# Kernel tuning notes

Measured on AMD Instinct MI355X. Metric: run time of the kernel, lower is better.

## Reference

```python
import jax, jax.numpy as jnp
import numpy as np
from jax import lax

B, C_IN, C_OUT, KK, KS = 8, 32, 64, 4, 3
D, H, W = 32, 64, 64
PAD = 1

def setup_inputs() -> dict:
    key = jax.random.key(0)
    ks = jax.random.split(key, 12)
    s = 0.02
    return {
        "x": jax.random.normal(ks[0], (B, C_IN, D, H, W), jnp.float32),
        # K candidate conv kernels and biases
        "weight": jax.random.normal(ks[1], (KK, C_OUT, C_IN, KS, KS, KS), jnp.float32) * s,
        "cbias": jnp.zeros((KK, C_OUT), jnp.float32),
        "temperature": jnp.float32(34.0),
        # attention key path: BN(affine, eval-mode) -> GELU -> 1x1 conv (linear)
        "bn1_g": jnp.ones((C_IN,), jnp.float32),
        "bn1_b": jnp.zeros((C_IN,), jnp.float32),
        "w1": jax.random.normal(ks[2], (C_IN, C_IN), jnp.float32) * s,
        "b1": jnp.zeros((C_IN,), jnp.float32),
        "bn2_g": jnp.ones((C_IN,), jnp.float32),
        "bn2_b": jnp.zeros((C_IN,), jnp.float32),
        "w2": jax.random.normal(ks[3], (C_IN, C_IN), jnp.float32) * s,
        "b2": jnp.zeros((C_IN,), jnp.float32),
        "bn3_g": jnp.ones((C_IN,), jnp.float32),
        "bn3_b": jnp.zeros((C_IN,), jnp.float32),
        "w3": jax.random.normal(ks[4], (KK, C_IN), jnp.float32) * s,
        "b3": jnp.zeros((KK,), jnp.float32),
    }

def _attention(p, temperature, bn1_g, bn1_b, w1, b1, bn2_g, bn2_b, w2, b2, bn3_g, bn3_b, w3, b3):
    # p: [B, C] pooled features. 1x1x1 convs on 1x1x1 maps == linear layers.
    gelu = lambda t: jax.nn.gelu(t, approximate=False)  # torch nn.GELU default is erf
    a = gelu(p * bn1_g + bn1_b)          # BN (eval: rm=0, rv=1) + GELU
    a = a @ w1.T + b1
    a = gelu(a * bn2_g + bn2_b)
    a = a @ w2.T + b2
    a = a + p                            # ResidualLayer (plain add)
    a = a * bn3_g + bn3_b
    logits = a @ w3.T + b3               # [B, K]
    return jax.nn.softmax(logits / temperature, axis=1)

def reference(x, weight, cbias, temperature, bn1_g, bn1_b, w1, b1,
              bn2_g, bn2_b, w2, b2, bn3_g, bn3_b, w3, b3):
    # x: [B, C_in, D, H, W]
    p = x.mean(axis=(2, 3, 4))  # AdaptiveAvgPool3d(1)
    attn = _attention(p, temperature, bn1_g, bn1_b, w1, b1,
                      bn2_g, bn2_b, w2, b2, bn3_g, bn3_b, w3, b3)  # [B, K]
    # per-sample aggregated kernels / bias
    agg_w = jnp.einsum('bk,koidhw->boidhw', attn, weight)  # [B, O, I, k, k, k]
    agg_b = attn @ cbias                                    # [B, O]
    # grouped-conv trick (groups=B) == per-sample conv3d -> vmap over batch
    def conv1(xi, wi):
        return lax.conv_general_dilated(
            xi[None], wi, window_strides=(1, 1, 1),
            padding=[(PAD, PAD)] * 3,
            dimension_numbers=('NCDHW', 'OIDHW', 'NCDHW'))[0]
    out = jax.vmap(conv1)(x, agg_w)  # [B, O, D, H, W]
    return out + agg_b[:, :, None, None, None]
```

## Files before the change

kernel.cpp:

```cpp
#include <hip/hip_runtime.h>
#include <hip/hip_bf16.h>
#include <math.h>

#define B_   8
#define CIN  32
#define COUT 64
#define KK_  4
#define DD   32
#define HH   64
#define WW   64
#define HW   (HH*WW)
#define DHW  (DD*HH*WW)

typedef __attribute__((ext_vector_type(8)))  short bf16x8;
typedef __attribute__((ext_vector_type(16))) float f32x16;

__device__ __forceinline__ unsigned short f2bf(float f) {
    union { float f; unsigned int u; } v; v.f = f;
    return (unsigned short)((v.u + 0x7FFFu + ((v.u >> 16) & 1u)) >> 16);
}
__device__ __forceinline__ float bf2f(unsigned short s) {
    union { unsigned int u; float f; } v; v.u = ((unsigned int)s) << 16;
    return v.f;
}
__device__ __forceinline__ void gll16(const void* g, void* l) {
    __builtin_amdgcn_global_load_lds(
        (const __attribute__((address_space(1))) void*)g,
        (__attribute__((address_space(3))) void*)l, 16, 0, 0);
}

__global__ __launch_bounds__(256) void transpose_kernel(const float* __restrict__ x,
                                                        unsigned short* __restrict__ xt) {
    const int t = threadIdx.x;
    const int r = t >> 6, w = t & 63;
    const int h = (blockIdx.x << 2) + r;
    const int d = blockIdx.y, b = blockIdx.z;

    const float* xb = x + (size_t)b*CIN*DHW + (size_t)d*HW + (size_t)h*WW + w;
    unsigned int packed[CIN/2];
    #pragma unroll
    for (int c2 = 0; c2 < CIN/2; ++c2) {
        unsigned int lo = f2bf(xb[(size_t)(2*c2)   * DHW]);
        unsigned int hi = f2bf(xb[(size_t)(2*c2+1) * DHW]);
        packed[c2] = lo | (hi << 16);
    }
    char* row = (char*)xt + (size_t)((b*DD + d)*HH + h) * 4096;
    #pragma unroll
    for (int q = 0; q < 4; ++q) {
        uint4 v = make_uint4(packed[4*q], packed[4*q+1], packed[4*q+2], packed[4*q+3]);
        *(uint4*)(row + q*1024 + (((w << 4)) ^ (q << 4))) = v;
    }
}

__global__ __launch_bounds__(256) void pool2_kernel(const unsigned short* __restrict__ xt,
                                                    float* __restrict__ pblk) {
    const int t = threadIdx.x;
    const int oct = t >> 6, wi = t & 63;
    const int d = blockIdx.x, b = blockIdx.y;
    const char* base = (const char*)xt + (size_t)((b*DD + d)*HH) * 4096 + oct*1024 + wi*16;
    float acc[8];
    #pragma unroll
    for (int j = 0; j < 8; ++j) acc[j] = 0.f;
    for (int h = 0; h < HH; ++h) {
        bf16x8 v = *(const bf16x8*)(base + (size_t)h * 4096);
        #pragma unroll
        for (int j = 0; j < 8; ++j) acc[j] += bf2f((unsigned short)v[j]);
    }
    #pragma unroll
    for (int off = 32; off > 0; off >>= 1) {
        #pragma unroll
        for (int j = 0; j < 8; ++j) acc[j] += __shfl_xor(acc[j], off);
    }
    if ((t & 63) == 0) {
        #pragma unroll
        for (int j = 0; j < 8; ++j)
            pblk[(b*DD + d)*CIN + oct*8 + j] = acc[j];
    }
}

__device__ __forceinline__ float gelu_erf(float v) {
    return 0.5f * v * (1.f + erff(v * 0.70710678118654752f));
}

__global__ void attn_kernel(const float* __restrict__ pblk,
                            const float* __restrict__ temperature,
                            const float* __restrict__ bn1_g, const float* __restrict__ bn1_b,
                            const float* __restrict__ w1,    const float* __restrict__ b1,
                            const float* __restrict__ bn2_g, const float* __restrict__ bn2_b,
                            const float* __restrict__ w2,    const float* __restrict__ b2,
                            const float* __restrict__ bn3_g, const float* __restrict__ bn3_b,
                            const float* __restrict__ w3,    const float* __restrict__ b3,
                            const float* __restrict__ cbias,
                            float* __restrict__ attn_out, float* __restrict__ aggb_out) {
    __shared__ float A[B_][CIN], A2[B_][CIN];
    __shared__ float L[B_][KK_], ATT[B_][KK_];
    const int t = threadIdx.x;
    const int b = t >> 5, c = t & 31;

    float pv = 0.f;
    for (int dd = 0; dd < DD; ++dd) pv += pblk[(b*DD + dd)*CIN + c];
    pv *= (1.f / (float)DHW);

    A[b][c] = gelu_erf(pv * bn1_g[c] + bn1_b[c]);
    __syncthreads();

    float s = b1[c];
    for (int j = 0; j < CIN; ++j) s += A[b][j] * w1[c*CIN + j];
    A2[b][c] = gelu_erf(s * bn2_g[c] + bn2_b[c]);
    __syncthreads();

    float s2 = b2[c];
    for (int j = 0; j < CIN; ++j) s2 += A2[b][j] * w2[c*CIN + j];
    s2 += pv;
    s2 = s2 * bn3_g[c] + bn3_b[c];
    __syncthreads();
    A[b][c] = s2;
    __syncthreads();

    if (c < KK_) {
        float lv = b3[c];
        for (int j = 0; j < CIN; ++j) lv += A[b][j] * w3[c*CIN + j];
        L[b][c] = lv;
    }
    __syncthreads();

    const float T = temperature[0];
    if (c < KK_) {
        float m = fmaxf(fmaxf(L[b][0], L[b][1]), fmaxf(L[b][2], L[b][3]));
        float e = expf((L[b][c] - m) / T);
        float den = 0.f;
        for (int j = 0; j < KK_; ++j) den += expf((L[b][j] - m) / T);
        float av = e / den;
        ATT[b][c] = av;
        attn_out[b*KK_ + c] = av;
    }
    __syncthreads();

    for (int o = c; o < COUT; o += CIN) {
        float sb = 0.f;
        for (int k = 0; k < KK_; ++k) sb += ATT[b][k] * cbias[k*COUT + o];
        aggb_out[b*COUT + o] = sb;
    }
}

__global__ void aggw_kernel(const float* __restrict__ weight,
                            const float* __restrict__ attn,
                            unsigned short* __restrict__ wt) {
    const int idx = blockIdx.x * 256 + threadIdx.x;
    const int ci   = idx & 31;
    const int co   = (idx >> 5) & 63;
    int r          = idx >> 11;
    const int kpos = r % 27;
    const int b    = r / 27;
    float s = 0.f;
    #pragma unroll
    for (int k = 0; k < KK_; ++k)
        s += attn[b*KK_ + k] * weight[((k*COUT + co)*CIN + ci)*27 + kpos];
    wt[idx] = f2bf(s);
}

__global__ __launch_bounds__(512, 2) void conv_mfma(const unsigned short* __restrict__ xt,
                                                    const unsigned short* __restrict__ wt,
                                                    const float* __restrict__ aggb,
                                                    float* __restrict__ out) {
    __shared__ char smem[36 * 4096];
    const int t    = threadIdx.x;
    const int lane = t & 63;
    const int wid  = t >> 6;
    const int wv   = wid & 1;
    const int hv   = wid >> 1;
    const int lw   = lane & 31, lh = lane >> 5;
    const int h0   = blockIdx.x << 2;
    const int d0   = blockIdx.y << 2;
    const int b    = blockIdx.z;

    const char* xb  = (const char*)xt + (size_t)(b*DD)*HH*4096;
    const char* wtb = (const char*)wt + (size_t)b * 27 * 4096;

    auto stage_row = [&](int zo, int ho) {
        const int zd = d0 - 1 + zo, yh = h0 - 1 + ho;
        char* dst = smem + (size_t)((zo*6 + ho) << 12);
        if ((unsigned)zd < DD && (unsigned)yh < HH) {
            const char* src = xb + (size_t)(zd*HH + yh)*4096 + lane*16;
            #pragma unroll
            for (int q = 0; q < 4; ++q) gll16(src + (q << 10), dst + (q << 10));
        } else {
            #pragma unroll
            for (int q = 0; q < 4; ++q)
                *(uint4*)(dst + (q << 10) + lane*16) = make_uint4(0u,0u,0u,0u);
        }
    };

    #pragma unroll
    for (int i = 0; i < 3; ++i) {
        const int rid = wid*3 + i;
        stage_row(rid % 6, rid / 6);
    }
    __syncthreads();
    if (wid < 6) stage_row(wid, 4);

    f32x16 acc[4][2];
    #pragma unroll
    for (int r = 0; r < 4; ++r) {
        acc[r][0] = (f32x16){};
        acc[r][1] = (f32x16){};
    }

    const int a_off = lw*64 + lh*16;
    const bf16x8 bz = {};
    const int o0 = lh, o1 = 2 + lh;

    #pragma unroll
    for (int kh = 0; kh < 3; ++kh) {
        if (kh == 1) {
            __syncthreads();
            if (wid < 6) stage_row(wid, 5);
        }
        if (kh == 2) __syncthreads();
        const int ho = hv + kh;
        #pragma unroll
        for (int kw = 0; kw < 3; ++kw) {
            const int wp  = (wv << 5) + lw + kw - 1;
            const bool oob = ((unsigned)wp >= (unsigned)WW);
            const int wpc = oob ? ((wp < 0) ? 0 : (WW - 1)) : wp;
            const int sw0 = (o0 << 10) + ((wpc << 4) ^ (o0 << 4));
            const int sw1 = (o1 << 10) + ((wpc << 4) ^ (o1 << 4));

            bf16x8 bc[6][2];
            #pragma unroll
            for (int zo = 0; zo < 6; ++zo) {
                const int rb = (zo*6 + ho) << 12;
                bf16x8 v0 = *(const bf16x8*)&smem[rb + sw0];
                bf16x8 v1 = *(const bf16x8*)&smem[rb + sw1];
                bc[zo][0] = oob ? bz : v0;
                bc[zo][1] = oob ? bz : v1;
            }
            #pragma unroll
            for (int kd = 0; kd < 3; ++kd) {
                const char* wk = wtb + (size_t)(((kd*3 + kh)*3 + kw) << 12);
                const bf16x8 a00 = *(const bf16x8*)(wk + a_off);
                const bf16x8 a01 = *(const bf16x8*)(wk + 32 + a_off);
                const bf16x8 a10 = *(const bf16x8*)(wk + 2048 + a_off);
                const bf16x8 a11 = *(const bf16x8*)(wk + 2048 + 32 + a_off);
                #pragma unroll
                for (int r = 0; r < 4; ++r) {
                    const int zo = r + kd;
                    acc[r][0] = __builtin_amdgcn_mfma_f32_32x32x16_bf16(a00, bc[zo][0], acc[r][0], 0, 0, 0);
                    acc[r][0] = __builtin_amdgcn_mfma_f32_32x32x16_bf16(a01, bc[zo][1], acc[r][0], 0, 0, 0);
                    acc[r][1] = __builtin_amdgcn_mfma_f32_32x32x16_bf16(a10, bc[zo][0], acc[r][1], 0, 0, 0);
                    acc[r][1] = __builtin_amdgcn_mfma_f32_32x32x16_bf16(a11, bc[zo][1], acc[r][1], 0, 0, 0);
                }
            }
        }
    }

    const float* ab = aggb + b*COUT;
    const int sp0 = (h0 + hv)*WW + (wv << 5) + lw;
    #pragma unroll
    for (int cb = 0; cb < 2; ++cb) {
        #pragma unroll
        for (int reg = 0; reg < 16; ++reg) {
            const int co = (cb << 5) + (reg & 3) + ((reg >> 2) << 3) + (lh << 2);
            const float bb = ab[co];
            float* oc = out + ((size_t)(b*COUT + co))*DHW + sp0;
            #pragma unroll
            for (int r = 0; r < 4; ++r)
                oc[(size_t)(d0 + r)*HW] = acc[r][cb][reg] + bb;
        }
    }
}

extern "C" void kernel_launch(void* const* d_in, const int* in_sizes, int n_in,
                              void* d_out, int out_size, void* d_ws, size_t ws_size,
                              hipStream_t stream) {
    const float* x           = (const float*)d_in[0];
    const float* weight      = (const float*)d_in[1];
    const float* cbias       = (const float*)d_in[2];
    const float* temperature = (const float*)d_in[3];
    const float* bn1_g       = (const float*)d_in[4];
    const float* bn1_b       = (const float*)d_in[5];
    const float* w1          = (const float*)d_in[6];
    const float* b1          = (const float*)d_in[7];
    const float* bn2_g       = (const float*)d_in[8];
    const float* bn2_b       = (const float*)d_in[9];
    const float* w2          = (const float*)d_in[10];
    const float* b2          = (const float*)d_in[11];
    const float* bn3_g       = (const float*)d_in[12];
    const float* bn3_b       = (const float*)d_in[13];
    const float* w3          = (const float*)d_in[14];
    const float* b3          = (const float*)d_in[15];
    float* out = (float*)d_out;

    char* ws = (char*)d_ws;
    float*          attn = (float*)(ws + 1024);
    float*          aggb = (float*)(ws + 2048);
    float*          pblk = (float*)(ws + 16384);
    unsigned short* wt   = (unsigned short*)(ws + 65536);
    unsigned short* xt   = (unsigned short*)(ws + (1u << 20));

    transpose_kernel<<<dim3(HH/4, DD, B_), 256, 0, stream>>>(x, xt);
    pool2_kernel<<<dim3(DD, B_), 256, 0, stream>>>(xt, pblk);
    attn_kernel<<<1, 256, 0, stream>>>(pblk, temperature,
                                       bn1_g, bn1_b, w1, b1,
                                       bn2_g, bn2_b, w2, b2,
                                       bn3_g, bn3_b, w3, b3,
                                       cbias, attn, aggb);
    aggw_kernel<<<(B_*27*COUT*CIN)/256, 256, 0, stream>>>(weight, attn, wt);
    conv_mfma<<<dim3(HH/4, DD/4, B_), 512, 0, stream>>>(xt, wt, aggb, out);
}
```

Before: 191.3 us.

## Retile conv to one H row per block with depth-split waves

The conv kernel now uses 256-thread blocks that each cover a single output H row and 4 depth slices. The 4 waves split the work by W half and depth pair, each accumulating 2 depth outputs instead of 4. Shared memory drops from 36 to 18 staged rows, loaded in one phase with a single barrier instead of the staged multi-barrier pipeline. This raises block count and occupancy and removes mid-loop syncs. In exchange the input halo is reloaded more often (3 rows per output row instead of 6 per 4), and register-level reuse of B fragments across depth falls.

```diff
diff --git a/kernel.cpp b/kernel.cpp
--- a/kernel.cpp
+++ b/kernel.cpp
@@ -159,18 +159,18 @@
     wt[idx] = f2bf(s);
 }
 
-__global__ __launch_bounds__(512, 2) void conv_mfma(const unsigned short* __restrict__ xt,
+__global__ __launch_bounds__(256, 2) void conv_mfma(const unsigned short* __restrict__ xt,
                                                     const unsigned short* __restrict__ wt,
                                                     const float* __restrict__ aggb,
                                                     float* __restrict__ out) {
-    __shared__ char smem[36 * 4096];
+    __shared__ char smem[18 * 4096];
     const int t    = threadIdx.x;
     const int lane = t & 63;
     const int wid  = t >> 6;
     const int wv   = wid & 1;
-    const int hv   = wid >> 1;
+    const int dv   = wid >> 1;
     const int lw   = lane & 31, lh = lane >> 5;
-    const int h0   = blockIdx.x << 2;
+    const int h    = blockIdx.x;
     const int d0   = blockIdx.y << 2;
     const int b    = blockIdx.z;
 
@@ -178,8 +178,8 @@
     const char* wtb = (const char*)wt + (size_t)b * 27 * 4096;
 
     auto stage_row = [&](int zo, int ho) {
-        const int zd = d0 - 1 + zo, yh = h0 - 1 + ho;
-        char* dst = smem + (size_t)((zo*6 + ho) << 12);
+        const int zd = d0 - 1 + zo, yh = h - 1 + ho;
+        char* dst = smem + (size_t)((zo*3 + ho) << 12);
         if ((unsigned)zd < DD && (unsigned)yh < HH) {
             const char* src = xb + (size_t)(zd*HH + yh)*4096 + lane*16;
             #pragma unroll
@@ -191,33 +191,20 @@
         }
     };
 
-    #pragma unroll
-    for (int i = 0; i < 3; ++i) {
-        const int rid = wid*3 + i;
-        stage_row(rid % 6, rid / 6);
-    }
-    __syncthreads();
-    if (wid < 6) stage_row(wid, 4);
-
-    f32x16 acc[4][2];
-    #pragma unroll
-    for (int r = 0; r < 4; ++r) {
-        acc[r][0] = (f32x16){};
-        acc[r][1] = (f32x16){};
-    }
+    for (int rid = wid; rid < 18; rid += 4)
+        stage_row(rid / 3, rid % 3);
+    __syncthreads();
+
+    f32x16 acc[2][2];
+    acc[0][0] = (f32x16){}; acc[0][1] = (f32x16){};
+    acc[1][0] = (f32x16){}; acc[1][1] = (f32x16){};
 
     const int a_off = lw*64 + lh*16;
+    const int o0 = lh, o1 = 2 + lh;
     const bf16x8 bz = {};
-    const int o0 = lh, o1 = 2 + lh;
 
     #pragma unroll
     for (int kh = 0; kh < 3; ++kh) {
-        if (kh == 1) {
-            __syncthreads();
-            if (wid < 6) stage_row(wid, 5);
-        }
-        if (kh == 2) __syncthreads();
-        const int ho = hv + kh;
         #pragma unroll
         for (int kw = 0; kw < 3; ++kw) {
             const int wp  = (wv << 5) + lw + kw - 1;
@@ -226,14 +213,14 @@
             const int sw0 = (o0 << 10) + ((wpc << 4) ^ (o0 << 4));
             const int sw1 = (o1 << 10) + ((wpc << 4) ^ (o1 << 4));
 
-            bf16x8 bc[6][2];
-            #pragma unroll
-            for (int zo = 0; zo < 6; ++zo) {
-                const int rb = (zo*6 + ho) << 12;
+            bf16x8 bc[4][2];
+            #pragma unroll
+            for (int j = 0; j < 4; ++j) {
+                const int rb = ((((dv << 1) + j)*3 + kh) << 12);
                 bf16x8 v0 = *(const bf16x8*)&smem[rb + sw0];
                 bf16x8 v1 = *(const bf16x8*)&smem[rb + sw1];
-                bc[zo][0] = oob ? bz : v0;
-                bc[zo][1] = oob ? bz : v1;
+                bc[j][0] = oob ? bz : v0;
+                bc[j][1] = oob ? bz : v1;
             }
             #pragma unroll
             for (int kd = 0; kd < 3; ++kd) {
@@ -243,19 +230,19 @@
                 const bf16x8 a10 = *(const bf16x8*)(wk + 2048 + a_off);
                 const bf16x8 a11 = *(const bf16x8*)(wk + 2048 + 32 + a_off);
                 #pragma unroll
-                for (int r = 0; r < 4; ++r) {
-                    const int zo = r + kd;
-                    acc[r][0] = __builtin_amdgcn_mfma_f32_32x32x16_bf16(a00, bc[zo][0], acc[r][0], 0, 0, 0);
-                    acc[r][0] = __builtin_amdgcn_mfma_f32_32x32x16_bf16(a01, bc[zo][1], acc[r][0], 0, 0, 0);
-                    acc[r][1] = __builtin_amdgcn_mfma_f32_32x32x16_bf16(a10, bc[zo][0], acc[r][1], 0, 0, 0);
-                    acc[r][1] = __builtin_amdgcn_mfma_f32_32x32x16_bf16(a11, bc[zo][1], acc[r][1], 0, 0, 0);
+                for (int r = 0; r < 2; ++r) {
+                    const int j = r + kd;
+                    acc[r][0] = __builtin_amdgcn_mfma_f32_32x32x16_bf16(a00, bc[j][0], acc[r][0], 0, 0, 0);
+                    acc[r][0] = __builtin_amdgcn_mfma_f32_32x32x16_bf16(a01, bc[j][1], acc[r][0], 0, 0, 0);
+                    acc[r][1] = __builtin_amdgcn_mfma_f32_32x32x16_bf16(a10, bc[j][0], acc[r][1], 0, 0, 0);
+                    acc[r][1] = __builtin_amdgcn_mfma_f32_32x32x16_bf16(a11, bc[j][1], acc[r][1], 0, 0, 0);
                 }
             }
         }
     }
 
     const float* ab = aggb + b*COUT;
-    const int sp0 = (h0 + hv)*WW + (wv << 5) + lw;
+    const int sp0 = h*WW + (wv << 5) + lw;
     #pragma unroll
     for (int cb = 0; cb < 2; ++cb) {
         #pragma unroll
@@ -264,8 +251,8 @@
             const float bb = ab[co];
             float* oc = out + ((size_t)(b*COUT + co))*DHW + sp0;
             #pragma unroll
-            for (int r = 0; r < 4; ++r)
-                oc[(size_t)(d0 + r)*HW] = acc[r][cb][reg] + bb;
+            for (int r = 0; r < 2; ++r)
+                oc[(size_t)(d0 + (dv << 1) + r)*HW] = acc[r][cb][reg] + bb;
         }
     }
 }
@@ -306,5 +293,5 @@
                                        bn3_g, bn3_b, w3, b3,
                                        cbias, attn, aggb);
     aggw_kernel<<<(B_*27*COUT*CIN)/256, 256, 0, stream>>>(weight, attn, wt);
-    conv_mfma<<<dim3(HH/4, DD/4, B_), 512, 0, stream>>>(xt, wt, aggb, out);
-}
+    conv_mfma<<<dim3(HH, DD/4, B_), 256, 0, stream>>>(xt, wt, aggb, out);
+}
```

After: 220.6 us. 15.3% more time.
